# Kernel tuning notes

Hardware: AMD Instinct MI355X
Metric: run time of the kernel (lower is better)

The kernel has to match this reference:

```python
import jax, jax.numpy as jnp
import numpy as np
from jax import lax

E, H, D = 1024, 16, 64          # embed_dim, num_heads, head_dim
B, T = 8, 64                    # batch, decode chunk
KV = 4096                       # kv_seq_len -> cache capacity 2*KV
START = 4096                    # start_pos (prefill already filled cache[:START])
THETA = 10000.0


def setup_inputs() -> dict:
    key = jax.random.key(0)
    kx, kck, kcv, kq, kk, kv, ko = jax.random.split(key, 7)
    s = 0.02
    return {
        "x": jax.random.normal(kx, (B, T, E), jnp.float32),
        "cache_keys": jax.random.normal(kck, (B, 2 * KV, H, D), jnp.float32),
        "cache_values": jax.random.normal(kcv, (B, 2 * KV, H, D), jnp.float32),
        "Wq": jax.random.normal(kq, (E, E), jnp.float32) * s,
        "Wk": jax.random.normal(kk, (E, E), jnp.float32) * s,
        "Wv": jax.random.normal(kv, (E, E), jnp.float32) * s,
        "Wo": jax.random.normal(ko, (E, E), jnp.float32) * s,
        "start_pos": START,
    }


def _rope_bug_faithful(x, start_pos):
    # x: (B, T, H, Dd). The source helper unpacks (B,H,T,D)=x.shape on a (B,T,H,D)
    # tensor, so rotation angles are indexed by HEAD index (positions
    # start_pos..start_pos+H-1) and broadcast over the time axis. Reproduced exactly.
    Bn, Tn, Hn, Dd = x.shape
    dh = Dd // 2
    inv_freq = 1.0 / (THETA ** (jnp.arange(dh, dtype=jnp.float32) / dh))
    pos = jnp.arange(Hn, dtype=jnp.float32) + jnp.float32(start_pos)  # (H,)
    ang = pos[:, None] * inv_freq[None, :]                            # (H, dh)
    cos = jnp.cos(ang)[None, None]                                    # (1,1,H,dh)
    sin = jnp.sin(ang)[None, None]
    xr = x.reshape(Bn, Tn, Hn, dh, 2)
    x0, x1 = xr[..., 0], xr[..., 1]
    o0 = x0 * cos - x1 * sin
    o1 = x0 * sin + x1 * cos
    return jnp.stack([o0, o1], axis=-1).reshape(Bn, Tn, Hn, Dd)


def reference(x, cache_keys, cache_values, Wq, Wk, Wv, Wo, start_pos):
    Bn, Tn, C = x.shape
    Hn, Dd = cache_keys.shape[2], cache_keys.shape[3]
    scale = 1.0 / np.sqrt(Dd).astype(np.float32)
    end = start_pos + Tn

    q = (x @ Wq).reshape(Bn, Tn, Hn, Dd)
    k = (x @ Wk).reshape(Bn, Tn, Hn, Dd)
    v = (x @ Wv).reshape(Bn, Tn, Hn, Dd)

    q = _rope_bug_faithful(q, start_pos)
    k = _rope_bug_faithful(k, start_pos)

    # cache append at dynamic offset (detached in source)
    ck = lax.dynamic_update_slice_in_dim(cache_keys, lax.stop_gradient(k), start_pos, axis=1)
    cv = lax.dynamic_update_slice_in_dim(cache_values, lax.stop_gradient(v), start_pos, axis=1)
    k_full = lax.stop_gradient(ck[:, :end])  # (B, S, H, D), S = end
    v_full = lax.stop_gradient(cv[:, :end])

    qh = q.transpose(0, 2, 1, 3)        # (B,H,T,D)
    kh = k_full.transpose(0, 2, 1, 3)   # (B,H,S,D)
    vh = v_full.transpose(0, 2, 1, 3)

    scores = jnp.einsum("bhtd,bhsd->bhts", qh, kh) * scale  # (B,H,T,S)
    i = jnp.arange(Tn)[:, None]
    j = jnp.arange(end)[None, :]
    allowed = j <= (start_pos + i)      # intended causal mask over cache span
    neg = jnp.finfo(scores.dtype).min
    scores = jnp.where(allowed[None, None], scores, neg)
    attn = jax.nn.softmax(scores, axis=-1)
    ctx = jnp.einsum("bhts,bhsd->bhtd", attn, vh)
    out = ctx.transpose(0, 2, 1, 3).reshape(Bn, Tn, C) @ Wo
    return out
```

## Files before the change

kernel.cpp:

```cpp
#include <hip/hip_runtime.h>
#include <hip/hip_bf16.h>
#include <math.h>

typedef __attribute__((ext_vector_type(8))) __bf16 bf16x8;
typedef __attribute__((ext_vector_type(4))) __bf16 bf16x4;
typedef __attribute__((ext_vector_type(4))) float f32x4;

#define EE 1024
#define HH 16
#define DD 64
#define BB 8
#define TT 64
#define NSPLIT 8

__device__ __forceinline__ f32x4 mfma16(bf16x8 a, bf16x8 b, f32x4 c) {
    return __builtin_amdgcn_mfma_f32_16x16x32_bf16(a, b, c, 0, 0, 0);
}

__global__ __launch_bounds__(256) void k_qkv(const float* __restrict__ x, const float* __restrict__ Wq,
                                             const float* __restrict__ Wk, const float* __restrict__ Wv,
                                             const int* __restrict__ sp_ptr,
                                             __bf16* __restrict__ qws, __bf16* __restrict__ knew,
                                             __bf16* __restrict__ vnew) {
    __shared__ __bf16 a_lds[64][72];
    __shared__ __bf16 b_lds[64][68];
    __shared__ float cs_l[32], sn_l[32];
    int xcd = blockIdx.x & 7, idx = blockIdx.x >> 3;
    int bn = xcd * 6 + idx % 6;
    int bm = idx / 6;
    int wsel = bn >> 4;
    int n0 = (bn & 15) * 64;
    int m0 = bm * 64;
    const float* W = (wsel == 0) ? Wq : (wsel == 1) ? Wk : Wv;
    int tid = threadIdx.x;
    int wv = tid >> 6, lane = tid & 63;
    int l16 = lane & 15, lhi = lane >> 4;
    int g = tid >> 4, m4 = (tid & 15) * 4;

    f32x4 acc[4];
#pragma unroll
    for (int f = 0; f < 4; ++f) acc[f] = (f32x4){0.f, 0.f, 0.f, 0.f};

    f32x4 areg[4], breg[4];
#pragma unroll
    for (int p = 0; p < 4; ++p)
        areg[p] = *(const f32x4*)&x[(size_t)(m0 + p * 16 + g) * EE + m4];
#pragma unroll
    for (int i = 0; i < 4; ++i)
        breg[i] = *(const f32x4*)&W[(size_t)(4 * g + i) * EE + n0 + m4];

    if (tid < 32) {
        int h = bn & 15;
        int sp = sp_ptr[0];
        float invf = powf(10000.0f, -(float)tid / 32.0f);
        float ang = (float)(sp + h) * invf;
        float s, c;
        sincosf(ang, &s, &c);
        cs_l[tid] = c;
        sn_l[tid] = s;
    }

    for (int kt = 0; kt < 16; ++kt) {
        __syncthreads();
#pragma unroll
        for (int p = 0; p < 4; ++p) {
            bf16x4 a4 = { (__bf16)areg[p][0], (__bf16)areg[p][1], (__bf16)areg[p][2], (__bf16)areg[p][3] };
            *(bf16x4*)&a_lds[p * 16 + g][m4] = a4;
        }
#pragma unroll
        for (int j = 0; j < 4; ++j) {
            bf16x4 t4 = { (__bf16)breg[0][j], (__bf16)breg[1][j], (__bf16)breg[2][j], (__bf16)breg[3][j] };
            *(bf16x4*)&b_lds[m4 + j][4 * g] = t4;
        }
        __syncthreads();
        if (kt < 15) {
            int ko = (kt + 1) * 64;
#pragma unroll
            for (int p = 0; p < 4; ++p)
                areg[p] = *(const f32x4*)&x[(size_t)(m0 + p * 16 + g) * EE + ko + m4];
#pragma unroll
            for (int i = 0; i < 4; ++i)
                breg[i] = *(const f32x4*)&W[(size_t)(ko + 4 * g + i) * EE + n0 + m4];
        }
        bf16x8 a0 = *(bf16x8*)&a_lds[wv * 16 + l16][lhi * 8];
        bf16x8 a1 = *(bf16x8*)&a_lds[wv * 16 + l16][32 + lhi * 8];
#pragma unroll
        for (int f = 0; f < 4; ++f) {
            bf16x8 b0 = *(bf16x8*)&b_lds[f * 16 + l16][lhi * 8];
            bf16x8 b1 = *(bf16x8*)&b_lds[f * 16 + l16][32 + lhi * 8];
            acc[f] = mfma16(a0, b0, acc[f]);
            acc[f] = mfma16(a1, b1, acc[f]);
        }
    }
    __bf16* dst = (wsel == 0) ? qws : (wsel == 1) ? knew : vnew;
    int h = bn & 15;
#pragma unroll
    for (int f = 0; f < 4; ++f) {
#pragma unroll
        for (int r = 0; r < 4; ++r) {
            float v = acc[f][r];
            int row = m0 + wv * 16 + lhi * 4 + r;
            int d = f * 16 + l16;
            float o = v;
            if (wsel < 2) {
                float other = __shfl_xor(v, 1);
                int pp = d >> 1;
                float c = cs_l[pp], s = sn_l[pp];
                o = ((d & 1) == 0) ? (v * c - other * s) : (other * s + v * c);
            }
            int b = row >> 6, t = row & 63;
            dst[((size_t)((b * HH + h) * TT + t)) * DD + d] = (__bf16)o;
        }
    }
}

__global__ __launch_bounds__(256, 4) void k_attn(const __bf16* __restrict__ qws, const __bf16* __restrict__ knew,
                                                 const __bf16* __restrict__ vnew,
                                                 const float* __restrict__ ck, const float* __restrict__ cv,
                                                 __bf16* __restrict__ Opart, float2* __restrict__ mlpart) {
    __shared__ __bf16 k_lds[64][72];
    __shared__ __bf16 vT_lds[64][68];
    __shared__ __bf16 p_lds[64][72];
    int bh = blockIdx.x >> 3, split = blockIdx.x & 7;
    int b = bh >> 4, h = bh & 15;
    int tid = threadIdx.x, wv = tid >> 6, lane = tid & 63;
    int l16 = lane & 15, lhi = lane >> 4;
    int g = tid >> 4, m4 = (tid & 15) * 4;

    bf16x8 qf0, qf1;
    {
        const __bf16* qp = qws + ((size_t)bh * TT + (wv * 16 + l16)) * DD;
        qf0 = *(const bf16x8*)&qp[lhi * 8];
        qf1 = *(const bf16x8*)&qp[32 + lhi * 8];
    }
    f32x4 acc[4];
#pragma unroll
    for (int f = 0; f < 4; ++f) acc[f] = (f32x4){0.f, 0.f, 0.f, 0.f};
    float l[4] = {0.f, 0.f, 0.f, 0.f};

    const float* ckb = ck + (size_t)b * 8192 * EE + h * DD;
    const float* cvb = cv + (size_t)b * 8192 * EE + h * DD;
    int s0 = split * 512;

    auto compute = [&](bool mask) {
        f32x4 sf[4];
#pragma unroll
        for (int f = 0; f < 4; ++f) {
            f32x4 z = (f32x4){0.f, 0.f, 0.f, 0.f};
            bf16x8 b0 = *(bf16x8*)&k_lds[f * 16 + l16][lhi * 8];
            bf16x8 b1 = *(bf16x8*)&k_lds[f * 16 + l16][32 + lhi * 8];
            z = mfma16(qf0, b0, z);
            z = mfma16(qf1, b1, z);
            sf[f] = z;
        }
        const float SC = 0.125f * 1.44269504f;
#pragma unroll
        for (int f = 0; f < 4; ++f) {
#pragma unroll
            for (int r = 0; r < 4; ++r) {
                float sv = sf[f][r] * SC;
                if (mask) {
                    int t_row = wv * 16 + lhi * 4 + r;
                    int s_loc = f * 16 + l16;
                    if (s_loc > t_row) sv = -1e30f;
                }
                float pv = exp2f(sv);
                sf[f][r] = pv;
                l[r] += pv;
            }
        }
#pragma unroll
        for (int f = 0; f < 4; ++f)
#pragma unroll
            for (int r = 0; r < 4; ++r)
                p_lds[wv * 16 + lhi * 4 + r][f * 16 + l16] = (__bf16)sf[f][r];
        bf16x8 pa0 = *(bf16x8*)&p_lds[wv * 16 + l16][lhi * 8];
        bf16x8 pa1 = *(bf16x8*)&p_lds[wv * 16 + l16][32 + lhi * 8];
#pragma unroll
        for (int f = 0; f < 4; ++f) {
            bf16x8 v0 = *(bf16x8*)&vT_lds[f * 16 + l16][lhi * 8];
            bf16x8 v1 = *(bf16x8*)&vT_lds[f * 16 + l16][32 + lhi * 8];
            acc[f] = mfma16(pa0, v0, acc[f]);
            acc[f] = mfma16(pa1, v1, acc[f]);
        }
    };

    f32x4 kreg[4], vreg[4];
#pragma unroll
    for (int p = 0; p < 4; ++p)
        kreg[p] = *(const f32x4*)&ckb[(size_t)(s0 + p * 16 + g) * EE + m4];
#pragma unroll
    for (int i = 0; i < 4; ++i)
        vreg[i] = *(const f32x4*)&cvb[(size_t)(s0 + 4 * g + i) * EE + m4];

    for (int it = 0; it < 8; ++it) {
#pragma unroll
        for (int p = 0; p < 4; ++p) {
            bf16x4 k4 = { (__bf16)kreg[p][0], (__bf16)kreg[p][1], (__bf16)kreg[p][2], (__bf16)kreg[p][3] };
            *(bf16x4*)&k_lds[p * 16 + g][m4] = k4;
        }
#pragma unroll
        for (int j = 0; j < 4; ++j) {
            bf16x4 tv = { (__bf16)vreg[0][j], (__bf16)vreg[1][j], (__bf16)vreg[2][j], (__bf16)vreg[3][j] };
            *(bf16x4*)&vT_lds[m4 + j][4 * g] = tv;
        }
        __syncthreads();
        if (it < 7) {
            int sb = s0 + (it + 1) * 64;
#pragma unroll
            for (int p = 0; p < 4; ++p)
                kreg[p] = *(const f32x4*)&ckb[(size_t)(sb + p * 16 + g) * EE + m4];
#pragma unroll
            for (int i = 0; i < 4; ++i)
                vreg[i] = *(const f32x4*)&cvb[(size_t)(sb + 4 * g + i) * EE + m4];
        }
        compute(false);
        __syncthreads();
    }

    if (split == 7) {
#pragma unroll
        for (int p = 0; p < 2; ++p) {
            int idx = p * 256 + tid;
            int r = idx >> 3, c8 = (idx & 7) * 8;
            *(bf16x8*)&k_lds[r][c8] = *(const bf16x8*)&knew[((size_t)bh * TT + r) * DD + c8];
            bf16x8 vf = *(const bf16x8*)&vnew[((size_t)bh * TT + r) * DD + c8];
#pragma unroll
            for (int j = 0; j < 8; ++j) vT_lds[c8 + j][r] = vf[j];
        }
        __syncthreads();
        compute(true);
    }

#pragma unroll
    for (int off = 1; off < 16; off <<= 1) {
#pragma unroll
        for (int r = 0; r < 4; ++r) l[r] += __shfl_xor(l[r], off);
    }

#pragma unroll
    for (int f = 0; f < 4; ++f)
#pragma unroll
        for (int r = 0; r < 4; ++r) {
            int t = wv * 16 + lhi * 4 + r;
            int d = f * 16 + l16;
            Opart[(((size_t)split * 128 + bh) * TT + t) * DD + d] = (__bf16)acc[f][r];
        }
    if (l16 == 0) {
#pragma unroll
        for (int r = 0; r < 4; ++r) {
            int t = wv * 16 + lhi * 4 + r;
            mlpart[((size_t)split * 128 + bh) * TT + t] = make_float2(0.f, l[r]);
        }
    }
}

__global__ __launch_bounds__(256) void k_combine(const __bf16* __restrict__ Opart, const float2* __restrict__ mlpart,
                                                 __bf16* __restrict__ ctxb) {
    int idx = blockIdx.x * 256 + threadIdx.x;
    int d = idx & 63, t = (idx >> 6) & 63, bh = idx >> 12;
    float ms[NSPLIT], ls[NSPLIT];
    float mg = -1e30f;
#pragma unroll
    for (int s = 0; s < NSPLIT; ++s) {
        float2 ml = mlpart[((size_t)s * 128 + bh) * TT + t];
        ms[s] = ml.x; ls[s] = ml.y;
        mg = fmaxf(mg, ms[s]);
    }
    float den = 0.f, num = 0.f;
#pragma unroll
    for (int s = 0; s < NSPLIT; ++s) {
        float w = __expf(ms[s] - mg);
        den += ls[s] * w;
        num += (float)Opart[(((size_t)s * 128 + bh) * TT + t) * DD + d] * w;
    }
    float ctx = num / den;
    int b = bh >> 4, hh = bh & 15;
    ctxb[(size_t)(b * TT + t) * EE + hh * DD + d] = (__bf16)ctx;
}

__global__ __launch_bounds__(256) void k_oproj(const __bf16* __restrict__ ctxb, const float* __restrict__ Wo,
                                               float* __restrict__ out) {
    __shared__ __bf16 a_lds[64][72];
    __shared__ __bf16 b_lds[64][68];
    int xcd = blockIdx.x & 7, idx = blockIdx.x >> 3;
    int bn = xcd * 2 + (idx & 1);
    int bm = idx >> 1;
    int n0 = bn * 64, m0 = bm * 64;
    int tid = threadIdx.x;
    int wv = tid >> 6, lane = tid & 63;
    int l16 = lane & 15, lhi = lane >> 4;
    int g = tid >> 4, m4 = (tid & 15) * 4;
    int r0 = tid >> 3, c8 = (tid & 7) * 8;
    f32x4 acc[4];
#pragma unroll
    for (int f = 0; f < 4; ++f) acc[f] = (f32x4){0.f, 0.f, 0.f, 0.f};

    bf16x8 ar0 = *(const bf16x8*)&ctxb[(size_t)(m0 + r0) * EE + c8];
    bf16x8 ar1 = *(const bf16x8*)&ctxb[(size_t)(m0 + 32 + r0) * EE + c8];
    f32x4 breg[4];
#pragma unroll
    for (int i = 0; i < 4; ++i)
        breg[i] = *(const f32x4*)&Wo[(size_t)(4 * g + i) * EE + n0 + m4];

    for (int kt = 0; kt < 16; ++kt) {
        __syncthreads();
        *(bf16x8*)&a_lds[r0][c8] = ar0;
        *(bf16x8*)&a_lds[32 + r0][c8] = ar1;
#pragma unroll
        for (int j = 0; j < 4; ++j) {
            bf16x4 t4 = { (__bf16)breg[0][j], (__bf16)breg[1][j], (__bf16)breg[2][j], (__bf16)breg[3][j] };
            *(bf16x4*)&b_lds[m4 + j][4 * g] = t4;
        }
        __syncthreads();
        if (kt < 15) {
            int ko = (kt + 1) * 64;
            ar0 = *(const bf16x8*)&ctxb[(size_t)(m0 + r0) * EE + ko + c8];
            ar1 = *(const bf16x8*)&ctxb[(size_t)(m0 + 32 + r0) * EE + ko + c8];
#pragma unroll
            for (int i = 0; i < 4; ++i)
                breg[i] = *(const f32x4*)&Wo[(size_t)(ko + 4 * g + i) * EE + n0 + m4];
        }
        bf16x8 a0 = *(bf16x8*)&a_lds[wv * 16 + l16][lhi * 8];
        bf16x8 a1 = *(bf16x8*)&a_lds[wv * 16 + l16][32 + lhi * 8];
#pragma unroll
        for (int f = 0; f < 4; ++f) {
            bf16x8 b0 = *(bf16x8*)&b_lds[f * 16 + l16][lhi * 8];
            bf16x8 b1 = *(bf16x8*)&b_lds[f * 16 + l16][32 + lhi * 8];
            acc[f] = mfma16(a0, b0, acc[f]);
            acc[f] = mfma16(a1, b1, acc[f]);
        }
    }
#pragma unroll
    for (int f = 0; f < 4; ++f)
#pragma unroll
        for (int r = 0; r < 4; ++r) {
            int row = m0 + wv * 16 + lhi * 4 + r;
            out[(size_t)row * EE + n0 + f * 16 + l16] = acc[f][r];
        }
}

extern "C" void kernel_launch(void* const* d_in, const int* in_sizes, int n_in,
                              void* d_out, int out_size, void* d_ws, size_t ws_size,
                              hipStream_t stream) {
    const float* x  = (const float*)d_in[0];
    const float* ck = (const float*)d_in[1];
    const float* cv = (const float*)d_in[2];
    const float* Wq = (const float*)d_in[3];
    const float* Wk = (const float*)d_in[4];
    const float* Wv = (const float*)d_in[5];
    const float* Wo = (const float*)d_in[6];
    const int* sp   = (const int*)d_in[7];
    float* out = (float*)d_out;

    char* p = (char*)d_ws;
    __bf16* qws = (__bf16*)p;           p += (size_t)524288 * 2;
    __bf16* knew = (__bf16*)p;          p += (size_t)524288 * 2;
    __bf16* vnew = (__bf16*)p;          p += (size_t)524288 * 2;
    __bf16* Opart = (__bf16*)p;         p += (size_t)NSPLIT * 128 * 64 * 64 * 2;
    float2* mlpart = (float2*)p;        p += (size_t)NSPLIT * 8192 * 8;
    __bf16* ctxb = (__bf16*)p;          p += (size_t)524288 * 2;

    k_qkv<<<384, 256, 0, stream>>>(x, Wq, Wk, Wv, sp, qws, knew, vnew);
    k_attn<<<BB * HH * NSPLIT, 256, 0, stream>>>(qws, knew, vnew, ck, cv, Opart, mlpart);
    k_combine<<<2048, 256, 0, stream>>>(Opart, mlpart, ctxb);
    k_oproj<<<128, 256, 0, stream>>>(ctxb, Wo, out);
}
```

Measured before the change: 94.98 us.

## Pre-transpose weights to bf16, simplify combine, move syncs after prefetch

Adds a prep kernel that transposes and converts all four weight matrices to bf16 on every call, so the QKV and output-projection GEMMs can load B tiles as contiguous bf16x8 rows with no in-register transpose. It also drops the unused max term from the split-softmax partials and vectorises the combine kernel to eight elements per thread. In the GEMM and attention loops, the barrier now sits after the next-tile prefetch is issued. The cost is an extra kernel launch plus a full extra read and write of the weights each call.

```diff
diff --git a/kernel.cpp b/kernel.cpp
--- a/kernel.cpp
+++ b/kernel.cpp
@@ -17,13 +17,41 @@
     return __builtin_amdgcn_mfma_f32_16x16x32_bf16(a, b, c, 0, 0, 0);
 }
 
-__global__ __launch_bounds__(256) void k_qkv(const float* __restrict__ x, const float* __restrict__ Wq,
-                                             const float* __restrict__ Wk, const float* __restrict__ Wv,
+__global__ __launch_bounds__(256) void k_prep(const float* __restrict__ Wq, const float* __restrict__ Wk,
+                                              const float* __restrict__ Wv, const float* __restrict__ Wo,
+                                              __bf16* __restrict__ WT) {
+    __shared__ float tile[64][68];
+    int bid = blockIdx.x;
+    int w = bid >> 8, tl = bid & 255;
+    int k0 = (tl >> 4) * 64, n0 = (tl & 15) * 64;
+    const float* W = (w == 0) ? Wq : (w == 1) ? Wk : (w == 2) ? Wv : Wo;
+    int tid = threadIdx.x;
+#pragma unroll
+    for (int p = 0; p < 4; ++p) {
+        int idx = p * 256 + tid;
+        int r = idx >> 4, c4 = (idx & 15) * 4;
+        float4 f = *(const float4*)&W[(size_t)(k0 + r) * EE + n0 + c4];
+        *(float4*)&tile[r][c4] = f;
+    }
+    __syncthreads();
+    __bf16* out = WT + (size_t)w * EE * EE;
+#pragma unroll
+    for (int p = 0; p < 2; ++p) {
+        int q = p * 256 + tid;
+        int r = q >> 3, c8 = (q & 7) * 8;
+        bf16x8 v;
+#pragma unroll
+        for (int j = 0; j < 8; ++j) v[j] = (__bf16)tile[c8 + j][r];
+        *(bf16x8*)&out[(size_t)(n0 + r) * EE + k0 + c8] = v;
+    }
+}
+
+__global__ __launch_bounds__(256) void k_qkv(const float* __restrict__ x, const __bf16* __restrict__ WT,
                                              const int* __restrict__ sp_ptr,
                                              __bf16* __restrict__ qws, __bf16* __restrict__ knew,
                                              __bf16* __restrict__ vnew) {
     __shared__ __bf16 a_lds[64][72];
-    __shared__ __bf16 b_lds[64][68];
+    __shared__ __bf16 b_lds[64][72];
     __shared__ float cs_l[32], sn_l[32];
     int xcd = blockIdx.x & 7, idx = blockIdx.x >> 3;
     int bn = xcd * 6 + idx % 6;
@@ -31,23 +59,24 @@
     int wsel = bn >> 4;
     int n0 = (bn & 15) * 64;
     int m0 = bm * 64;
-    const float* W = (wsel == 0) ? Wq : (wsel == 1) ? Wk : Wv;
+    const __bf16* Wt = WT + (size_t)wsel * EE * EE;
     int tid = threadIdx.x;
     int wv = tid >> 6, lane = tid & 63;
     int l16 = lane & 15, lhi = lane >> 4;
     int g = tid >> 4, m4 = (tid & 15) * 4;
+    int r0 = tid >> 3, c8 = (tid & 7) * 8;
 
     f32x4 acc[4];
 #pragma unroll
     for (int f = 0; f < 4; ++f) acc[f] = (f32x4){0.f, 0.f, 0.f, 0.f};
 
-    f32x4 areg[4], breg[4];
+    f32x4 areg[4];
+    bf16x8 br0, br1;
 #pragma unroll
     for (int p = 0; p < 4; ++p)
         areg[p] = *(const f32x4*)&x[(size_t)(m0 + p * 16 + g) * EE + m4];
-#pragma unroll
-    for (int i = 0; i < 4; ++i)
-        breg[i] = *(const f32x4*)&W[(size_t)(4 * g + i) * EE + n0 + m4];
+    br0 = *(const bf16x8*)&Wt[(size_t)(n0 + r0) * EE + c8];
+    br1 = *(const bf16x8*)&Wt[(size_t)(n0 + 32 + r0) * EE + c8];
 
     if (tid < 32) {
         int h = bn & 15;
@@ -67,21 +96,17 @@
             bf16x4 a4 = { (__bf16)areg[p][0], (__bf16)areg[p][1], (__bf16)areg[p][2], (__bf16)areg[p][3] };
             *(bf16x4*)&a_lds[p * 16 + g][m4] = a4;
         }
-#pragma unroll
-        for (int j = 0; j < 4; ++j) {
-            bf16x4 t4 = { (__bf16)breg[0][j], (__bf16)breg[1][j], (__bf16)breg[2][j], (__bf16)breg[3][j] };
-            *(bf16x4*)&b_lds[m4 + j][4 * g] = t4;
-        }
-        __syncthreads();
+        *(bf16x8*)&b_lds[r0][c8] = br0;
+        *(bf16x8*)&b_lds[32 + r0][c8] = br1;
         if (kt < 15) {
             int ko = (kt + 1) * 64;
 #pragma unroll
             for (int p = 0; p < 4; ++p)
                 areg[p] = *(const f32x4*)&x[(size_t)(m0 + p * 16 + g) * EE + ko + m4];
-#pragma unroll
-            for (int i = 0; i < 4; ++i)
-                breg[i] = *(const f32x4*)&W[(size_t)(ko + 4 * g + i) * EE + n0 + m4];
-        }
+            br0 = *(const bf16x8*)&Wt[(size_t)(n0 + r0) * EE + ko + c8];
+            br1 = *(const bf16x8*)&Wt[(size_t)(n0 + 32 + r0) * EE + ko + c8];
+        }
+        __syncthreads();
         bf16x8 a0 = *(bf16x8*)&a_lds[wv * 16 + l16][lhi * 8];
         bf16x8 a1 = *(bf16x8*)&a_lds[wv * 16 + l16][32 + lhi * 8];
 #pragma unroll
@@ -117,7 +142,7 @@
 __global__ __launch_bounds__(256, 4) void k_attn(const __bf16* __restrict__ qws, const __bf16* __restrict__ knew,
                                                  const __bf16* __restrict__ vnew,
                                                  const float* __restrict__ ck, const float* __restrict__ cv,
-                                                 __bf16* __restrict__ Opart, float2* __restrict__ mlpart) {
+                                                 __bf16* __restrict__ Opart, float* __restrict__ lpart) {
     __shared__ __bf16 k_lds[64][72];
     __shared__ __bf16 vT_lds[64][68];
     __shared__ __bf16 p_lds[64][72];
@@ -204,7 +229,6 @@
             bf16x4 tv = { (__bf16)vreg[0][j], (__bf16)vreg[1][j], (__bf16)vreg[2][j], (__bf16)vreg[3][j] };
             *(bf16x4*)&vT_lds[m4 + j][4 * g] = tv;
         }
-        __syncthreads();
         if (it < 7) {
             int sb = s0 + (it + 1) * 64;
 #pragma unroll
@@ -214,6 +238,7 @@
             for (int i = 0; i < 4; ++i)
                 vreg[i] = *(const f32x4*)&cvb[(size_t)(sb + 4 * g + i) * EE + m4];
         }
+        __syncthreads();
         compute(false);
         __syncthreads();
     }
@@ -250,39 +275,37 @@
 #pragma unroll
         for (int r = 0; r < 4; ++r) {
             int t = wv * 16 + lhi * 4 + r;
-            mlpart[((size_t)split * 128 + bh) * TT + t] = make_float2(0.f, l[r]);
-        }
-    }
-}
-
-__global__ __launch_bounds__(256) void k_combine(const __bf16* __restrict__ Opart, const float2* __restrict__ mlpart,
+            lpart[((size_t)split * 128 + bh) * TT + t] = l[r];
+        }
+    }
+}
+
+__global__ __launch_bounds__(256) void k_combine(const __bf16* __restrict__ Opart, const float* __restrict__ lpart,
                                                  __bf16* __restrict__ ctxb) {
     int idx = blockIdx.x * 256 + threadIdx.x;
-    int d = idx & 63, t = (idx >> 6) & 63, bh = idx >> 12;
-    float ms[NSPLIT], ls[NSPLIT];
-    float mg = -1e30f;
+    int d8 = idx & 7, t = (idx >> 3) & 63, bh = idx >> 9;
+    float den = 0.f, num[8];
+#pragma unroll
+    for (int j = 0; j < 8; ++j) num[j] = 0.f;
 #pragma unroll
     for (int s = 0; s < NSPLIT; ++s) {
-        float2 ml = mlpart[((size_t)s * 128 + bh) * TT + t];
-        ms[s] = ml.x; ls[s] = ml.y;
-        mg = fmaxf(mg, ms[s]);
-    }
-    float den = 0.f, num = 0.f;
-#pragma unroll
-    for (int s = 0; s < NSPLIT; ++s) {
-        float w = __expf(ms[s] - mg);
-        den += ls[s] * w;
-        num += (float)Opart[(((size_t)s * 128 + bh) * TT + t) * DD + d] * w;
-    }
-    float ctx = num / den;
-    int b = bh >> 4, hh = bh & 15;
-    ctxb[(size_t)(b * TT + t) * EE + hh * DD + d] = (__bf16)ctx;
-}
-
-__global__ __launch_bounds__(256) void k_oproj(const __bf16* __restrict__ ctxb, const float* __restrict__ Wo,
+        den += lpart[((size_t)s * 128 + bh) * TT + t];
+        bf16x8 o = *(const bf16x8*)&Opart[(((size_t)s * 128 + bh) * TT + t) * DD + d8 * 8];
+#pragma unroll
+        for (int j = 0; j < 8; ++j) num[j] += (float)o[j];
+    }
+    float inv = 1.0f / den;
+    bf16x8 c;
+#pragma unroll
+    for (int j = 0; j < 8; ++j) c[j] = (__bf16)(num[j] * inv);
+    int b = bh >> 4, h = bh & 15;
+    *(bf16x8*)&ctxb[(size_t)(b * TT + t) * EE + h * DD + d8 * 8] = c;
+}
+
+__global__ __launch_bounds__(256) void k_oproj(const __bf16* __restrict__ ctxb, const __bf16* __restrict__ WoT,
                                                float* __restrict__ out) {
     __shared__ __bf16 a_lds[64][72];
-    __shared__ __bf16 b_lds[64][68];
+    __shared__ __bf16 b_lds[64][72];
     int xcd = blockIdx.x & 7, idx = blockIdx.x >> 3;
     int bn = xcd * 2 + (idx & 1);
     int bm = idx >> 1;
@@ -290,7 +313,6 @@
     int tid = threadIdx.x;
     int wv = tid >> 6, lane = tid & 63;
     int l16 = lane & 15, lhi = lane >> 4;
-    int g = tid >> 4, m4 = (tid & 15) * 4;
     int r0 = tid >> 3, c8 = (tid & 7) * 8;
     f32x4 acc[4];
 #pragma unroll
@@ -298,29 +320,23 @@
 
     bf16x8 ar0 = *(const bf16x8*)&ctxb[(size_t)(m0 + r0) * EE + c8];
     bf16x8 ar1 = *(const bf16x8*)&ctxb[(size_t)(m0 + 32 + r0) * EE + c8];
-    f32x4 breg[4];
-#pragma unroll
-    for (int i = 0; i < 4; ++i)
-        breg[i] = *(const f32x4*)&Wo[(size_t)(4 * g + i) * EE + n0 + m4];
+    bf16x8 br0 = *(const bf16x8*)&WoT[(size_t)(n0 + r0) * EE + c8];
+    bf16x8 br1 = *(const bf16x8*)&WoT[(size_t)(n0 + 32 + r0) * EE + c8];
 
     for (int kt = 0; kt < 16; ++kt) {
         __syncthreads();
         *(bf16x8*)&a_lds[r0][c8] = ar0;
         *(bf16x8*)&a_lds[32 + r0][c8] = ar1;
-#pragma unroll
-        for (int j = 0; j < 4; ++j) {
-            bf16x4 t4 = { (__bf16)breg[0][j], (__bf16)breg[1][j], (__bf16)breg[2][j], (__bf16)breg[3][j] };
-            *(bf16x4*)&b_lds[m4 + j][4 * g] = t4;
-        }
-        __syncthreads();
+        *(bf16x8*)&b_lds[r0][c8] = br0;
+        *(bf16x8*)&b_lds[32 + r0][c8] = br1;
         if (kt < 15) {
             int ko = (kt + 1) * 64;
             ar0 = *(const bf16x8*)&ctxb[(size_t)(m0 + r0) * EE + ko + c8];
             ar1 = *(const bf16x8*)&ctxb[(size_t)(m0 + 32 + r0) * EE + ko + c8];
-#pragma unroll
-            for (int i = 0; i < 4; ++i)
-                breg[i] = *(const f32x4*)&Wo[(size_t)(ko + 4 * g + i) * EE + n0 + m4];
-        }
+            br0 = *(const bf16x8*)&WoT[(size_t)(n0 + r0) * EE + ko + c8];
+            br1 = *(const bf16x8*)&WoT[(size_t)(n0 + 32 + r0) * EE + ko + c8];
+        }
+        __syncthreads();
         bf16x8 a0 = *(bf16x8*)&a_lds[wv * 16 + l16][lhi * 8];
         bf16x8 a1 = *(bf16x8*)&a_lds[wv * 16 + l16][32 + lhi * 8];
 #pragma unroll
@@ -354,15 +370,17 @@
     float* out = (float*)d_out;
 
     char* p = (char*)d_ws;
+    __bf16* WT = (__bf16*)p;            p += (size_t)4 * 1024 * 1024 * 2;
     __bf16* qws = (__bf16*)p;           p += (size_t)524288 * 2;
     __bf16* knew = (__bf16*)p;          p += (size_t)524288 * 2;
     __bf16* vnew = (__bf16*)p;          p += (size_t)524288 * 2;
     __bf16* Opart = (__bf16*)p;         p += (size_t)NSPLIT * 128 * 64 * 64 * 2;
-    float2* mlpart = (float2*)p;        p += (size_t)NSPLIT * 8192 * 8;
+    float* lpart = (float*)p;           p += (size_t)NSPLIT * 8192 * 4;
     __bf16* ctxb = (__bf16*)p;          p += (size_t)524288 * 2;
 
-    k_qkv<<<384, 256, 0, stream>>>(x, Wq, Wk, Wv, sp, qws, knew, vnew);
-    k_attn<<<BB * HH * NSPLIT, 256, 0, stream>>>(qws, knew, vnew, ck, cv, Opart, mlpart);
-    k_combine<<<2048, 256, 0, stream>>>(Opart, mlpart, ctxb);
-    k_oproj<<<128, 256, 0, stream>>>(ctxb, Wo, out);
-}
+    k_prep<<<1024, 256, 0, stream>>>(Wq, Wk, Wv, Wo, WT);
+    k_qkv<<<384, 256, 0, stream>>>(x, WT, sp, qws, knew, vnew);
+    k_attn<<<BB * HH * NSPLIT, 256, 0, stream>>>(qws, knew, vnew, ck, cv, Opart, lpart);
+    k_combine<<<256, 256, 0, stream>>>(Opart, lpart, ctxb);
+    k_oproj<<<128, 256, 0, stream>>>(ctxb, WT + (size_t)3 * 1024 * 1024, out);
+}
```

Result: faster. 84.37 us (median of 2 runs) (-11.2%).
